# Optimization experiments

Hardware: AMD Instinct MI355X
Metric: run time of the kernel (lower is better)

Reference implementation:

```python
import jax, jax.numpy as jnp
import numpy as np

N_NODES = 100000
N_EDGES = 1600000
IN_DIM = 128
HID = 32
BN_EPS = 1e-5


def setup_inputs() -> dict:
    key = jax.random.key(0)
    ks = jax.random.split(key, 6)
    x = jax.random.normal(ks[0], (N_NODES, IN_DIM), dtype=jnp.float32)
    edge_index = jax.random.randint(ks[1], (2, N_EDGES), 0, N_NODES, dtype=jnp.int64)
    # Glorot-ish scaled weights (PyG GCNConv uses glorot init)
    W1 = jax.random.normal(ks[2], (IN_DIM, HID), dtype=jnp.float32) * (1.0 / np.sqrt(IN_DIM))
    b1 = jnp.zeros((HID,), dtype=jnp.float32)
    gamma = jnp.ones((HID,), dtype=jnp.float32)
    beta = jnp.zeros((HID,), dtype=jnp.float32)
    W2 = jax.random.normal(ks[3], (HID, HID), dtype=jnp.float32) * (1.0 / np.sqrt(HID))
    b2 = jnp.zeros((HID,), dtype=jnp.float32)
    return {"x": x, "edge_index": edge_index, "W1": W1, "b1": b1,
            "gamma": gamma, "beta": beta, "W2": W2, "b2": b2}


def _gcn_conv(x, src, dst, norm, W, b, n_nodes):
    # GCNConv: out = D^{-1/2}(A+I)D^{-1/2} (x W) + b
    h = x @ W                                   # [N, F_out]
    msg = h[src] * norm[:, None]                # gather + scale, [E+N, F_out]
    out = jax.ops.segment_sum(msg, dst, num_segments=n_nodes)  # scatter-add
    return out + b


def _gcn_norm(edge_index, n_nodes):
    # add self loops, symmetric normalization
    loop = jnp.arange(n_nodes, dtype=edge_index.dtype)
    src = jnp.concatenate([edge_index[0], loop])
    dst = jnp.concatenate([edge_index[1], loop])
    deg = jax.ops.segment_sum(jnp.ones_like(dst, dtype=jnp.float32), dst,
                              num_segments=n_nodes)
    dinv = jax.lax.rsqrt(jnp.maximum(deg, 1.0))  # deg >= 1 due to self loops
    norm = dinv[src] * dinv[dst]
    return src, dst, norm


def reference(x, edge_index, W1, b1, gamma, beta, W2, b2):
    n = x.shape[0]
    src, dst, norm = _gcn_norm(edge_index, n)
    h = _gcn_conv(x, src, dst, norm, W1, b1, n)
    # BatchNorm over nodes (training-mode batch statistics, biased variance)
    mean = jnp.mean(h, axis=0)
    var = jnp.mean((h - mean) ** 2, axis=0)
    h = (h - mean) * jax.lax.rsqrt(var + BN_EPS) * gamma + beta
    h = jax.nn.relu(h)
    # dropout is identity in eval mode
    out = _gcn_conv(h, src, dst, norm, W2, b2, n)
    return out
```

## Files before the change

### kernel.cpp

```cpp
#include <hip/hip_runtime.h>
#include <hip/hip_bf16.h>

#define INDIM 128
#define HID 32
#define BN_EPS 1e-5f
#define BSH 8
#define MAXB 512
#define PCHUNK 4096

__global__ void ge_detect(const int* __restrict__ ei, int* __restrict__ flag) {
    int is64 = 1;
    for (int i = 1; i < 128; i += 2)
        if (ei[i] != 0) { is64 = 0; break; }
    *flag = is64;
}

__global__ __launch_bounds__(256) void ge_bhist(const int* __restrict__ ei,
                                                const int* __restrict__ flag,
                                                unsigned* __restrict__ bcnt, int E, int nb) {
    __shared__ unsigned h[MAXB];
    int t = threadIdx.x;
    h[t] = 0; h[t + 256] = 0;
    __syncthreads();
    int is64 = *flag;
    int stride = gridDim.x * 256;
    if (is64) {
        const unsigned long long* p = (const unsigned long long*)ei;
        for (int e = blockIdx.x * 256 + t; e < E; e += stride)
            atomicAdd(&h[((unsigned)p[E + e]) >> BSH], 1u);
    } else {
        for (int e = blockIdx.x * 256 + t; e < E; e += stride)
            atomicAdd(&h[((unsigned)ei[E + e]) >> BSH], 1u);
    }
    __syncthreads();
    for (int b = t; b < nb; b += 256)
        if (h[b]) atomicAdd(&bcnt[b], h[b]);
}

__global__ void ge_bscan(const unsigned* __restrict__ bcnt, unsigned* __restrict__ bstart,
                         unsigned* __restrict__ bwptr, int nb, int E) {
    __shared__ unsigned s[MAXB];
    int t = threadIdx.x;
    unsigned v = (t < nb) ? bcnt[t] : 0u;
    s[t] = v;
    __syncthreads();
    for (int off = 1; off < MAXB; off <<= 1) {
        unsigned u = (t >= off) ? s[t - off] : 0u;
        __syncthreads();
        s[t] += u;
        __syncthreads();
    }
    if (t < nb) { unsigned ex = s[t] - v; bstart[t] = ex; bwptr[t] = ex; }
    if (t == 0) bstart[nb] = (unsigned)E;
}

__global__ __launch_bounds__(256) void ge_bpart(const int* __restrict__ ei,
                                                const int* __restrict__ flag,
                                                unsigned* __restrict__ bwptr,
                                                uint2* __restrict__ ebuf, int E, int nb) {
    __shared__ uint2 es[PCHUNK];
    __shared__ unsigned cnt[MAXB];
    __shared__ unsigned base[MAXB];
    int t = threadIdx.x;
    int start = blockIdx.x * PCHUNK;
    int len = min(PCHUNK, E - start);
    cnt[t] = 0; cnt[t + 256] = 0;
    __syncthreads();
    int is64 = *flag;
    if (is64) {
        const unsigned long long* p = (const unsigned long long*)ei;
        for (int i = t; i < len; i += 256) {
            unsigned s = (unsigned)p[start + i];
            unsigned d = (unsigned)p[E + start + i];
            es[i] = make_uint2(s, d);
            atomicAdd(&cnt[d >> BSH], 1u);
        }
    } else {
        for (int i = t; i < len; i += 256) {
            unsigned s = (unsigned)ei[start + i];
            unsigned d = (unsigned)ei[E + start + i];
            es[i] = make_uint2(s, d);
            atomicAdd(&cnt[d >> BSH], 1u);
        }
    }
    __syncthreads();
    for (int b = t; b < nb; b += 256) {
        unsigned c = cnt[b];
        base[b] = c ? atomicAdd(&bwptr[b], c) : 0u;
        cnt[b] = 0;
    }
    __syncthreads();
    for (int i = t; i < len; i += 256) {
        uint2 e = es[i];
        unsigned b = e.y >> BSH;
        unsigned pos = base[b] + atomicAdd(&cnt[b], 1u);
        ebuf[pos] = e;
    }
}

__global__ __launch_bounds__(256) void ge_bcsr(const uint2* __restrict__ ebuf,
                                               const unsigned* __restrict__ bstart,
                                               unsigned* __restrict__ rowst,
                                               unsigned* __restrict__ deg,
                                               float* __restrict__ dinv,
                                               unsigned* __restrict__ col, int n) {
    __shared__ unsigned cnt[256];
    __shared__ unsigned pos[256];
    int b = blockIdx.x;
    int t = threadIdx.x;
    unsigned bs = bstart[b], be = bstart[b + 1];
    cnt[t] = 0;
    __syncthreads();
    for (unsigned i = bs + t; i < be; i += 256)
        atomicAdd(&cnt[ebuf[i].y & 255u], 1u);
    __syncthreads();
    unsigned v = cnt[t];
    pos[t] = v;
    __syncthreads();
    for (int off = 1; off < 256; off <<= 1) {
        unsigned u = (t >= off) ? pos[t - off] : 0u;
        __syncthreads();
        pos[t] += u;
        __syncthreads();
    }
    unsigned ex = pos[t] - v;
    int node = (b << BSH) + t;
    if (node < n) {
        rowst[node] = bs + ex;
        deg[node] = v;
        dinv[node] = rsqrtf((float)(v + 1u));
    }
    __syncthreads();
    pos[t] = ex;
    cnt[t] = 0;
    __syncthreads();
    for (unsigned i = bs + t; i < be; i += 256) {
        uint2 e = ebuf[i];
        unsigned d = e.y & 255u;
        unsigned o = atomicAdd(&cnt[d], 1u);
        col[bs + pos[d] + o] = e.x;
    }
}

__global__ __launch_bounds__(256) void ge_gemm1(const float* __restrict__ x,
                                                const float* __restrict__ W1,
                                                const float* __restrict__ dinv,
                                                float* __restrict__ g1, int n) {
    int node = blockIdx.x * blockDim.x + threadIdx.x;
    if (node >= n) return;
    float acc[HID];
#pragma unroll
    for (int c = 0; c < HID; c++) acc[c] = 0.f;
    const float4* xr = (const float4*)(x + (size_t)node * INDIM);
    for (int k4 = 0; k4 < INDIM / 4; k4++) {
        float4 xv = xr[k4];
        const float* w = W1 + (size_t)k4 * 4 * HID;
#pragma unroll
        for (int kk = 0; kk < 4; kk++) {
            float xk = (&xv.x)[kk];
#pragma unroll
            for (int c = 0; c < HID; c++) acc[c] = fmaf(xk, w[kk * HID + c], acc[c]);
        }
    }
    float dv = dinv[node];
    float4* out = (float4*)(g1 + (size_t)node * HID);
#pragma unroll
    for (int c4 = 0; c4 < HID / 4; c4++) {
        float4 o;
        o.x = acc[c4 * 4 + 0] * dv;
        o.y = acc[c4 * 4 + 1] * dv;
        o.z = acc[c4 * 4 + 2] * dv;
        o.w = acc[c4 * 4 + 3] * dv;
        out[c4] = o;
    }
}

__global__ __launch_bounds__(256) void ge_gather(const float* __restrict__ g,
                                                 const unsigned* __restrict__ row_start,
                                                 const unsigned* __restrict__ deg,
                                                 const unsigned* __restrict__ col,
                                                 const float* __restrict__ dinv,
                                                 const float* __restrict__ bias,
                                                 float* __restrict__ out, int n) {
    int idx = blockIdx.x * blockDim.x + threadIdx.x;
    int node = idx >> 5;
    int c = idx & 31;
    if (node >= n) return;
    unsigned start = row_start[node];
    unsigned len = deg[node];
    float acc = g[(size_t)node * HID + c];
    unsigned j = 0;
    for (; j + 4 <= len; j += 4) {
        unsigned c0 = col[start + j + 0];
        unsigned c1 = col[start + j + 1];
        unsigned c2 = col[start + j + 2];
        unsigned c3 = col[start + j + 3];
        float v0 = g[(size_t)c0 * HID + c];
        float v1 = g[(size_t)c1 * HID + c];
        float v2 = g[(size_t)c2 * HID + c];
        float v3 = g[(size_t)c3 * HID + c];
        acc += v0 + v1 + v2 + v3;
    }
    for (; j < len; j++) acc += g[(size_t)col[start + j] * HID + c];
    out[(size_t)node * HID + c] = dinv[node] * acc + bias[c];
}

__global__ __launch_bounds__(256) void ge_bnstats(const float* __restrict__ h1,
                                                  float* __restrict__ bnsum,
                                                  float* __restrict__ bnsumsq, int n) {
    int t = threadIdx.x;
    int c = t & 31;
    int rg = t >> 5;
    float s = 0.f, q = 0.f;
    for (int r = blockIdx.x * 8 + rg; r < n; r += gridDim.x * 8) {
        float v = h1[(size_t)r * HID + c];
        s += v;
        q += v * v;
    }
    __shared__ float Ls[256], Lq[256];
    Ls[t] = s; Lq[t] = q;
    __syncthreads();
    for (int off = 128; off >= 32; off >>= 1) {
        if (t < off) { Ls[t] += Ls[t + off]; Lq[t] += Lq[t + off]; }
        __syncthreads();
    }
    if (t < 32) {
        atomicAdd(&bnsum[t], Ls[t]);
        atomicAdd(&bnsumsq[t], Lq[t]);
    }
}

__global__ void ge_bnfinal(const float* __restrict__ bnsum, const float* __restrict__ bnsumsq,
                           const float* __restrict__ gamma, const float* __restrict__ beta,
                           float* __restrict__ ab, int n) {
    int c = threadIdx.x;
    if (c >= HID) return;
    float inv_n = 1.f / (float)n;
    float mean = bnsum[c] * inv_n;
    float var = fmaxf(bnsumsq[c] * inv_n - mean * mean, 0.f);
    float inv = rsqrtf(var + BN_EPS);
    float a = gamma[c] * inv;
    ab[c] = a;
    ab[HID + c] = beta[c] - mean * a;
}

__global__ __launch_bounds__(256) void ge_gemm2(const float* __restrict__ h1,
                                                const float* __restrict__ W2,
                                                const float* __restrict__ ab,
                                                const float* __restrict__ dinv,
                                                float* __restrict__ g2, int n) {
    int node = blockIdx.x * blockDim.x + threadIdx.x;
    if (node >= n) return;
    float p[HID];
    const float4* hr = (const float4*)(h1 + (size_t)node * HID);
#pragma unroll
    for (int k4 = 0; k4 < HID / 4; k4++) {
        float4 v = hr[k4];
#pragma unroll
        for (int kk = 0; kk < 4; kk++) {
            int k = k4 * 4 + kk;
            p[k] = fmaxf(fmaf(ab[k], (&v.x)[kk], ab[HID + k]), 0.f);
        }
    }
    float acc[HID];
#pragma unroll
    for (int c = 0; c < HID; c++) acc[c] = 0.f;
#pragma unroll
    for (int k = 0; k < HID; k++) {
        float pk = p[k];
        const float* w = W2 + (size_t)k * HID;
#pragma unroll
        for (int c = 0; c < HID; c++) acc[c] = fmaf(pk, w[c], acc[c]);
    }
    float dv = dinv[node];
    float4* out = (float4*)(g2 + (size_t)node * HID);
#pragma unroll
    for (int c4 = 0; c4 < HID / 4; c4++) {
        float4 o;
        o.x = acc[c4 * 4 + 0] * dv;
        o.y = acc[c4 * 4 + 1] * dv;
        o.z = acc[c4 * 4 + 2] * dv;
        o.w = acc[c4 * 4 + 3] * dv;
        out[c4] = o;
    }
}

extern "C" void kernel_launch(void* const* d_in, const int* in_sizes, int n_in,
                              void* d_out, int out_size, void* d_ws, size_t ws_size,
                              hipStream_t stream) {
    const float* x     = (const float*)d_in[0];
    const int*   ei    = (const int*)d_in[1];
    const float* W1    = (const float*)d_in[2];
    const float* b1    = (const float*)d_in[3];
    const float* gamma = (const float*)d_in[4];
    const float* beta  = (const float*)d_in[5];
    const float* W2    = (const float*)d_in[6];
    const float* b2    = (const float*)d_in[7];
    float* outp = (float*)d_out;

    const int n = in_sizes[0] / INDIM;
    const int E = in_sizes[1] / 2;
    const int nb = (n + 255) >> 8;

    char* w = (char*)d_ws;
    size_t off = 0;
    auto nxt = [&](size_t b) -> void* {
        void* p = w + off;
        off += (b + 255) & ~(size_t)255;
        return p;
    };
    unsigned* bcnt    = (unsigned*)nxt(MAXB * 4);
    float*    bnsum   = (float*)nxt(HID * 4);
    float*    bnsumsq = (float*)nxt(HID * 4);
    size_t zero_end = off;
    int*      flag    = (int*)nxt(16);
    unsigned* bstart  = (unsigned*)nxt((MAXB + 1) * 4);
    unsigned* bwptr   = (unsigned*)nxt(MAXB * 4);
    unsigned* deg     = (unsigned*)nxt((size_t)n * 4);
    unsigned* rowst   = (unsigned*)nxt((size_t)n * 4);
    float*    dinv    = (float*)nxt((size_t)n * 4);
    float*    ab      = (float*)nxt(2 * HID * 4);
    unsigned* colx    = (unsigned*)nxt((size_t)E * 4);
    float*    g1      = (float*)nxt((size_t)n * HID * 4);
    float*    h1      = (float*)nxt((size_t)n * HID * 4);
    float*    g2      = g1;
    uint2*    ebuf    = (uint2*)d_out;

    hipMemsetAsync(d_ws, 0, zero_end, stream);

    ge_detect<<<1, 1, 0, stream>>>(ei, flag);

    ge_bhist<<<512, 256, 0, stream>>>(ei, flag, bcnt, E, nb);
    ge_bscan<<<1, MAXB, 0, stream>>>(bcnt, bstart, bwptr, nb, E);
    ge_bpart<<<(E + PCHUNK - 1) / PCHUNK, 256, 0, stream>>>(ei, flag, bwptr, ebuf, E, nb);
    ge_bcsr<<<nb, 256, 0, stream>>>(ebuf, bstart, rowst, deg, dinv, colx, n);

    ge_gemm1<<<(n + 255) / 256, 256, 0, stream>>>(x, W1, dinv, g1, n);

    int gbl = ((n * 32) + 255) / 256;
    ge_gather<<<gbl, 256, 0, stream>>>(g1, rowst, deg, colx, dinv, b1, h1, n);

    ge_bnstats<<<1024, 256, 0, stream>>>(h1, bnsum, bnsumsq, n);
    ge_bnfinal<<<1, 64, 0, stream>>>(bnsum, bnsumsq, gamma, beta, ab, n);

    ge_gemm2<<<(n + 255) / 256, 256, 0, stream>>>(h1, W2, ab, dinv, g2, n);

    ge_gather<<<gbl, 256, 0, stream>>>(g2, rowst, deg, colx, dinv, b2, outp, n);
}
```

Before: 302.1 us.

## Store intermediate features as bf16, fuse BN stats into gather, inline index-width detection

Intermediate node feature buffers (g1, h1, g2) are now stored as packed bf16 pairs, halving the bytes moved by the random-access gathers and the GEMM epilogues. Each gather thread handles two channels. The first gather also accumulates the batch-norm sum and sum of squares, spreading its atomics over 64 partial slots, which removes the separate stats kernel. The single-thread detect kernel is replaced by a per-block shared-memory check inside the histogram and partition kernels. The cost is reduced precision of intermediate features compared with the fp32 reference.

New measurement: 275.1 us. 8.9% less time.

```diff
diff --git a/kernel.cpp b/kernel.cpp
--- a/kernel.cpp
+++ b/kernel.cpp
@@ -3,26 +3,39 @@
 
 #define INDIM 128
 #define HID 32
+#define HID2 16
 #define BN_EPS 1e-5f
 #define BSH 8
 #define MAXB 512
 #define PCHUNK 4096
-
-__global__ void ge_detect(const int* __restrict__ ei, int* __restrict__ flag) {
-    int is64 = 1;
-    for (int i = 1; i < 128; i += 2)
-        if (ei[i] != 0) { is64 = 0; break; }
-    *flag = is64;
+#define BNP 64
+
+static __device__ __forceinline__ unsigned pk2bf(float lo, float hi) {
+    unsigned a = __float_as_uint(lo);
+    unsigned b = __float_as_uint(hi);
+    a = (a + 0x7fffu + ((a >> 16) & 1u)) >> 16;
+    b = (b + 0x7fffu + ((b >> 16) & 1u)) & 0xffff0000u;
+    return a | b;
+}
+static __device__ __forceinline__ float bflo(unsigned u) { return __uint_as_float(u << 16); }
+static __device__ __forceinline__ float bfhi(unsigned u) { return __uint_as_float(u & 0xffff0000u); }
+
+static __device__ __forceinline__ int detect_is64(const int* __restrict__ ei, int t) {
+    __shared__ int sh;
+    if (t == 0) sh = 1;
+    __syncthreads();
+    if (t < 64 && ei[2 * t + 1] != 0) sh = 0;
+    __syncthreads();
+    return sh;
 }
 
 __global__ __launch_bounds__(256) void ge_bhist(const int* __restrict__ ei,
-                                                const int* __restrict__ flag,
                                                 unsigned* __restrict__ bcnt, int E, int nb) {
+    int t = threadIdx.x;
+    int is64 = detect_is64(ei, t);
     __shared__ unsigned h[MAXB];
-    int t = threadIdx.x;
     h[t] = 0; h[t + 256] = 0;
     __syncthreads();
-    int is64 = *flag;
     int stride = gridDim.x * 256;
     if (is64) {
         const unsigned long long* p = (const unsigned long long*)ei;
@@ -55,18 +68,17 @@
 }
 
 __global__ __launch_bounds__(256) void ge_bpart(const int* __restrict__ ei,
-                                                const int* __restrict__ flag,
                                                 unsigned* __restrict__ bwptr,
                                                 uint2* __restrict__ ebuf, int E, int nb) {
+    int t = threadIdx.x;
+    int is64 = detect_is64(ei, t);
     __shared__ uint2 es[PCHUNK];
     __shared__ unsigned cnt[MAXB];
     __shared__ unsigned base[MAXB];
-    int t = threadIdx.x;
     int start = blockIdx.x * PCHUNK;
     int len = min(PCHUNK, E - start);
     cnt[t] = 0; cnt[t + 256] = 0;
     __syncthreads();
-    int is64 = *flag;
     if (is64) {
         const unsigned long long* p = (const unsigned long long*)ei;
         for (int i = t; i < len; i += 256) {
@@ -145,13 +157,14 @@
 __global__ __launch_bounds__(256) void ge_gemm1(const float* __restrict__ x,
                                                 const float* __restrict__ W1,
                                                 const float* __restrict__ dinv,
-                                                float* __restrict__ g1, int n) {
+                                                unsigned* __restrict__ g1, int n) {
     int node = blockIdx.x * blockDim.x + threadIdx.x;
     if (node >= n) return;
     float acc[HID];
 #pragma unroll
     for (int c = 0; c < HID; c++) acc[c] = 0.f;
     const float4* xr = (const float4*)(x + (size_t)node * INDIM);
+#pragma unroll 4
     for (int k4 = 0; k4 < INDIM / 4; k4++) {
         float4 xv = xr[k4];
         const float* w = W1 + (size_t)k4 * 4 * HID;
@@ -163,103 +176,118 @@
         }
     }
     float dv = dinv[node];
-    float4* out = (float4*)(g1 + (size_t)node * HID);
-#pragma unroll
-    for (int c4 = 0; c4 < HID / 4; c4++) {
-        float4 o;
-        o.x = acc[c4 * 4 + 0] * dv;
-        o.y = acc[c4 * 4 + 1] * dv;
-        o.z = acc[c4 * 4 + 2] * dv;
-        o.w = acc[c4 * 4 + 3] * dv;
-        out[c4] = o;
-    }
-}
-
-__global__ __launch_bounds__(256) void ge_gather(const float* __restrict__ g,
-                                                 const unsigned* __restrict__ row_start,
+    unsigned og[HID2];
+#pragma unroll
+    for (int i = 0; i < HID2; i++) og[i] = pk2bf(acc[2 * i] * dv, acc[2 * i + 1] * dv);
+    uint4* o4 = (uint4*)(g1 + (size_t)node * HID2);
+#pragma unroll
+    for (int i = 0; i < 4; i++)
+        o4[i] = make_uint4(og[4 * i], og[4 * i + 1], og[4 * i + 2], og[4 * i + 3]);
+}
+
+template<bool OUT_BF16, bool FUSE_BN>
+__global__ __launch_bounds__(256) void ge_gather(const unsigned* __restrict__ g,
+                                                 const unsigned* __restrict__ rowst,
                                                  const unsigned* __restrict__ deg,
                                                  const unsigned* __restrict__ col,
                                                  const float* __restrict__ dinv,
                                                  const float* __restrict__ bias,
-                                                 float* __restrict__ out, int n) {
-    int idx = blockIdx.x * blockDim.x + threadIdx.x;
-    int node = idx >> 5;
-    int c = idx & 31;
-    if (node >= n) return;
-    unsigned start = row_start[node];
-    unsigned len = deg[node];
-    float acc = g[(size_t)node * HID + c];
-    unsigned j = 0;
-    for (; j + 4 <= len; j += 4) {
-        unsigned c0 = col[start + j + 0];
-        unsigned c1 = col[start + j + 1];
-        unsigned c2 = col[start + j + 2];
-        unsigned c3 = col[start + j + 3];
-        float v0 = g[(size_t)c0 * HID + c];
-        float v1 = g[(size_t)c1 * HID + c];
-        float v2 = g[(size_t)c2 * HID + c];
-        float v3 = g[(size_t)c3 * HID + c];
-        acc += v0 + v1 + v2 + v3;
-    }
-    for (; j < len; j++) acc += g[(size_t)col[start + j] * HID + c];
-    out[(size_t)node * HID + c] = dinv[node] * acc + bias[c];
-}
-
-__global__ __launch_bounds__(256) void ge_bnstats(const float* __restrict__ h1,
-                                                  float* __restrict__ bnsum,
-                                                  float* __restrict__ bnsumsq, int n) {
-    int t = threadIdx.x;
-    int c = t & 31;
-    int rg = t >> 5;
-    float s = 0.f, q = 0.f;
-    for (int r = blockIdx.x * 8 + rg; r < n; r += gridDim.x * 8) {
-        float v = h1[(size_t)r * HID + c];
-        s += v;
-        q += v * v;
-    }
-    __shared__ float Ls[256], Lq[256];
-    Ls[t] = s; Lq[t] = q;
-    __syncthreads();
-    for (int off = 128; off >= 32; off >>= 1) {
-        if (t < off) { Ls[t] += Ls[t + off]; Lq[t] += Lq[t + off]; }
-        __syncthreads();
-    }
-    if (t < 32) {
-        atomicAdd(&bnsum[t], Ls[t]);
-        atomicAdd(&bnsumsq[t], Lq[t]);
-    }
-}
-
-__global__ void ge_bnfinal(const float* __restrict__ bnsum, const float* __restrict__ bnsumsq,
+                                                 unsigned* __restrict__ outb,
+                                                 float* __restrict__ outf,
+                                                 float* __restrict__ bnsum,
+                                                 float* __restrict__ bnsq, int n) {
+    int t = threadIdx.x;
+    int idx = blockIdx.x * 256 + t;
+    int node = idx >> 4, cp = idx & 15;
+    float h0 = 0.f, h1v = 0.f;
+    if (node < n) {
+        unsigned self = g[(size_t)node * HID2 + cp];
+        float a0 = bflo(self), a1 = bfhi(self);
+        unsigned st = rowst[node], len = deg[node];
+        unsigned j = 0;
+        for (; j + 4 <= len; j += 4) {
+            unsigned c0 = col[st + j + 0];
+            unsigned c1 = col[st + j + 1];
+            unsigned c2 = col[st + j + 2];
+            unsigned c3 = col[st + j + 3];
+            unsigned u0 = g[(size_t)c0 * HID2 + cp];
+            unsigned u1 = g[(size_t)c1 * HID2 + cp];
+            unsigned u2 = g[(size_t)c2 * HID2 + cp];
+            unsigned u3 = g[(size_t)c3 * HID2 + cp];
+            a0 += (bflo(u0) + bflo(u1)) + (bflo(u2) + bflo(u3));
+            a1 += (bfhi(u0) + bfhi(u1)) + (bfhi(u2) + bfhi(u3));
+        }
+        for (; j < len; j++) {
+            unsigned u = g[(size_t)col[st + j] * HID2 + cp];
+            a0 += bflo(u); a1 += bfhi(u);
+        }
+        float dv = dinv[node];
+        float2 bb = ((const float2*)bias)[cp];
+        h0 = fmaf(dv, a0, bb.x);
+        h1v = fmaf(dv, a1, bb.y);
+        if (OUT_BF16) {
+            outb[(size_t)node * HID2 + cp] = pk2bf(h0, h1v);
+        } else {
+            float2 o; o.x = h0; o.y = h1v;
+            ((float2*)outf)[(size_t)node * HID2 + cp] = o;
+        }
+    }
+    if (FUSE_BN) {
+        __shared__ float4 red[256];
+        red[t] = make_float4(h0, h0 * h0, h1v, h1v * h1v);
+        __syncthreads();
+        for (int off = 128; off >= 16; off >>= 1) {
+            if (t < off) {
+                float4 a = red[t], b = red[t + off];
+                red[t] = make_float4(a.x + b.x, a.y + b.y, a.z + b.z, a.w + b.w);
+            }
+            __syncthreads();
+        }
+        if (t < 16) {
+            float4 v = red[t];
+            int p = blockIdx.x & (BNP - 1);
+            atomicAdd(&bnsum[p * HID + 2 * t + 0], v.x);
+            atomicAdd(&bnsq [p * HID + 2 * t + 0], v.y);
+            atomicAdd(&bnsum[p * HID + 2 * t + 1], v.z);
+            atomicAdd(&bnsq [p * HID + 2 * t + 1], v.w);
+        }
+    }
+}
+
+__global__ void ge_bnfinal(const float* __restrict__ bnsum, const float* __restrict__ bnsq,
                            const float* __restrict__ gamma, const float* __restrict__ beta,
                            float* __restrict__ ab, int n) {
     int c = threadIdx.x;
     if (c >= HID) return;
+    float s = 0.f, q = 0.f;
+    for (int p = 0; p < BNP; p++) { s += bnsum[p * HID + c]; q += bnsq[p * HID + c]; }
     float inv_n = 1.f / (float)n;
-    float mean = bnsum[c] * inv_n;
-    float var = fmaxf(bnsumsq[c] * inv_n - mean * mean, 0.f);
-    float inv = rsqrtf(var + BN_EPS);
-    float a = gamma[c] * inv;
+    float mean = s * inv_n;
+    float var = fmaxf(q * inv_n - mean * mean, 0.f);
+    float iv = rsqrtf(var + BN_EPS);
+    float a = gamma[c] * iv;
     ab[c] = a;
     ab[HID + c] = beta[c] - mean * a;
 }
 
-__global__ __launch_bounds__(256) void ge_gemm2(const float* __restrict__ h1,
+__global__ __launch_bounds__(256) void ge_gemm2(const unsigned* __restrict__ h1,
                                                 const float* __restrict__ W2,
                                                 const float* __restrict__ ab,
                                                 const float* __restrict__ dinv,
-                                                float* __restrict__ g2, int n) {
+                                                unsigned* __restrict__ g2, int n) {
     int node = blockIdx.x * blockDim.x + threadIdx.x;
     if (node >= n) return;
     float p[HID];
-    const float4* hr = (const float4*)(h1 + (size_t)node * HID);
-#pragma unroll
-    for (int k4 = 0; k4 < HID / 4; k4++) {
-        float4 v = hr[k4];
-#pragma unroll
-        for (int kk = 0; kk < 4; kk++) {
-            int k = k4 * 4 + kk;
-            p[k] = fmaxf(fmaf(ab[k], (&v.x)[kk], ab[HID + k]), 0.f);
+    const uint4* hr = (const uint4*)(h1 + (size_t)node * HID2);
+#pragma unroll
+    for (int i4 = 0; i4 < 4; i4++) {
+        uint4 u4 = hr[i4];
+        const unsigned* u = &u4.x;
+#pragma unroll
+        for (int j = 0; j < 4; j++) {
+            int k0 = (i4 * 4 + j) * 2, k1 = k0 + 1;
+            p[k0] = fmaxf(fmaf(ab[k0], bflo(u[j]), ab[HID + k0]), 0.f);
+            p[k1] = fmaxf(fmaf(ab[k1], bfhi(u[j]), ab[HID + k1]), 0.f);
         }
     }
     float acc[HID];
@@ -273,16 +301,13 @@
         for (int c = 0; c < HID; c++) acc[c] = fmaf(pk, w[c], acc[c]);
     }
     float dv = dinv[node];
-    float4* out = (float4*)(g2 + (size_t)node * HID);
-#pragma unroll
-    for (int c4 = 0; c4 < HID / 4; c4++) {
-        float4 o;
-        o.x = acc[c4 * 4 + 0] * dv;
-        o.y = acc[c4 * 4 + 1] * dv;
-        o.z = acc[c4 * 4 + 2] * dv;
-        o.w = acc[c4 * 4 + 3] * dv;
-        out[c4] = o;
-    }
+    unsigned og[HID2];
+#pragma unroll
+    for (int i = 0; i < HID2; i++) og[i] = pk2bf(acc[2 * i] * dv, acc[2 * i + 1] * dv);
+    uint4* o4 = (uint4*)(g2 + (size_t)node * HID2);
+#pragma unroll
+    for (int i = 0; i < 4; i++)
+        o4[i] = make_uint4(og[4 * i], og[4 * i + 1], og[4 * i + 2], og[4 * i + 3]);
 }
 
 extern "C" void kernel_launch(void* const* d_in, const int* in_sizes, int n_in,
@@ -310,10 +335,9 @@
         return p;
     };
     unsigned* bcnt    = (unsigned*)nxt(MAXB * 4);
-    float*    bnsum   = (float*)nxt(HID * 4);
-    float*    bnsumsq = (float*)nxt(HID * 4);
+    float*    bnsum   = (float*)nxt(BNP * HID * 4);
+    float*    bnsq    = (float*)nxt(BNP * HID * 4);
     size_t zero_end = off;
-    int*      flag    = (int*)nxt(16);
     unsigned* bstart  = (unsigned*)nxt((MAXB + 1) * 4);
     unsigned* bwptr   = (unsigned*)nxt(MAXB * 4);
     unsigned* deg     = (unsigned*)nxt((size_t)n * 4);
@@ -321,29 +345,27 @@
     float*    dinv    = (float*)nxt((size_t)n * 4);
     float*    ab      = (float*)nxt(2 * HID * 4);
     unsigned* colx    = (unsigned*)nxt((size_t)E * 4);
-    float*    g1      = (float*)nxt((size_t)n * HID * 4);
-    float*    h1      = (float*)nxt((size_t)n * HID * 4);
-    float*    g2      = g1;
+    unsigned* g1      = (unsigned*)nxt((size_t)n * HID2 * 4);
+    unsigned* h1      = (unsigned*)nxt((size_t)n * HID2 * 4);
+    unsigned* g2      = g1;
     uint2*    ebuf    = (uint2*)d_out;
 
     hipMemsetAsync(d_ws, 0, zero_end, stream);
 
-    ge_detect<<<1, 1, 0, stream>>>(ei, flag);
-
-    ge_bhist<<<512, 256, 0, stream>>>(ei, flag, bcnt, E, nb);
+    ge_bhist<<<512, 256, 0, stream>>>(ei, bcnt, E, nb);
     ge_bscan<<<1, MAXB, 0, stream>>>(bcnt, bstart, bwptr, nb, E);
-    ge_bpart<<<(E + PCHUNK - 1) / PCHUNK, 256, 0, stream>>>(ei, flag, bwptr, ebuf, E, nb);
+    ge_bpart<<<(E + PCHUNK - 1) / PCHUNK, 256, 0, stream>>>(ei, bwptr, ebuf, E, nb);
     ge_bcsr<<<nb, 256, 0, stream>>>(ebuf, bstart, rowst, deg, dinv, colx, n);
 
     ge_gemm1<<<(n + 255) / 256, 256, 0, stream>>>(x, W1, dinv, g1, n);
 
-    int gbl = ((n * 32) + 255) / 256;
-    ge_gather<<<gbl, 256, 0, stream>>>(g1, rowst, deg, colx, dinv, b1, h1, n);
-
-    ge_bnstats<<<1024, 256, 0, stream>>>(h1, bnsum, bnsumsq, n);
-    ge_bnfinal<<<1, 64, 0, stream>>>(bnsum, bnsumsq, gamma, beta, ab, n);
+    int gbl = ((n * HID2) + 255) / 256;
+    ge_gather<true, true><<<gbl, 256, 0, stream>>>(g1, rowst, deg, colx, dinv, b1,
+                                                   h1, nullptr, bnsum, bnsq, n);
+    ge_bnfinal<<<1, 64, 0, stream>>>(bnsum, bnsq, gamma, beta, ab, n);
 
     ge_gemm2<<<(n + 255) / 256, 256, 0, stream>>>(h1, W2, ab, dinv, g2, n);
 
-    ge_gather<<<gbl, 256, 0, stream>>>(g2, rowst, deg, colx, dinv, b2, outp, n);
-}
+    ge_gather<false, false><<<gbl, 256, 0, stream>>>(g2, rowst, deg, colx, dinv, b2,
+                                                     nullptr, outp, nullptr, nullptr, n);
+}
```
